# Kernel tuning notes

Measured on AMD Instinct MI355X. Metric: run time of the kernel, lower is better.

Reference implementation:

```python
import jax, jax.numpy as jnp
import numpy as np
import math

B, N, C = 16, 4096, 256
WS = 8            # window_size
NH = 8            # num_heads
HD = C // NH      # head_dim = 32
LK = 32           # linformer compressed length
G = 16            # global bank tokens


def setup_inputs() -> dict:
    key = jax.random.key(0)
    ks = jax.random.split(key, 10)
    x = jax.random.normal(ks[0], (B, N, C), dtype=jnp.float32)
    W_qkv = jax.random.normal(ks[1], (C, 3 * C), dtype=jnp.float32) * 0.02
    b_qkv = jnp.zeros((3 * C,), dtype=jnp.float32)
    E_k = jax.random.normal(ks[2], (WS * WS, LK), dtype=jnp.float32) * 0.02
    E_v = jax.random.normal(ks[3], (WS * WS, LK), dtype=jnp.float32) * 0.02
    k_bank = jax.random.normal(ks[4], (G, C), dtype=jnp.float32)
    v_bank = jax.random.normal(ks[5], (G, C), dtype=jnp.float32)
    W_proj = jax.random.normal(ks[6], (C, C), dtype=jnp.float32) * 0.02
    b_proj = jnp.zeros((C,), dtype=jnp.float32)
    return {"x": x, "W_qkv": W_qkv, "b_qkv": b_qkv, "E_k": E_k, "E_v": E_v,
            "k_bank": k_bank, "v_bank": v_bank, "W_proj": W_proj, "b_proj": b_proj,
            "window_size": WS, "num_heads": NH}


def reference(x, W_qkv, b_qkv, E_k, E_v, k_bank, v_bank, W_proj, b_proj, window_size, num_heads):
    Bb, Nn, Cc = x.shape
    Hs = int(math.isqrt(Nn))          # H = W = sqrt(N), divisible by window_size here
    ws = window_size
    nh = Hs // ws                      # windows per side
    hd = Cc // num_heads
    NW = ws * ws                       # tokens per window

    # ---- window partition: [B,N,C] -> [BW, NW, C]
    xw = x.reshape(Bb, nh, ws, nh, ws, Cc).transpose(0, 1, 3, 2, 4, 5)
    xw = xw.reshape(Bb * nh * nh, NW, Cc)
    BW = xw.shape[0]

    # ---- qkv projection and head split: (3, BW, H, NW, hd)
    qkv = (xw @ W_qkv + b_qkv).reshape(BW, NW, 3, num_heads, hd)
    qkv = qkv.transpose(2, 0, 3, 1, 4)
    q, k, v = qkv[0], qkv[1], qkv[2]

    # ---- Linformer KV compression: NW == seq_len (no pad branch)
    k_c = jnp.einsum('nk,bhnd->bhkd', E_k, k)   # [BW,H,LK,hd]
    v_c = jnp.einsum('nk,bhnd->bhkd', E_v, v)

    # ---- global memory bank, broadcast to all windows: [BW,H,G,hd]
    Gt = k_bank.shape[0]
    kb = jnp.broadcast_to(k_bank.reshape(Gt, num_heads, hd).transpose(1, 0, 2)[None],
                          (BW, num_heads, Gt, hd))
    vb = jnp.broadcast_to(v_bank.reshape(Gt, num_heads, hd).transpose(1, 0, 2)[None],
                          (BW, num_heads, Gt, hd))

    k_full = jnp.concatenate([k_c, kb], axis=2)  # [BW,H,LK+G,hd]
    v_full = jnp.concatenate([v_c, vb], axis=2)

    # ---- SDPA (dropout_p = 0)
    scale = 1.0 / math.sqrt(hd)
    scores = jnp.einsum('bhqd,bhkd->bhqk', q, k_full) * scale
    attn = jax.nn.softmax(scores, axis=-1)
    out = jnp.einsum('bhqk,bhkd->bhqd', attn, v_full)     # [BW,H,NW,hd]

    out = out.transpose(0, 2, 1, 3).reshape(BW, NW, Cc)
    out = out @ W_proj + b_proj

    # ---- window reverse: [BW,NW,C] -> [B,N,C]
    out = out.reshape(Bb, nh, nh, ws, ws, Cc).transpose(0, 1, 3, 2, 4, 5)
    out = out.reshape(Bb, Hs * Hs, Cc)
    return out
```

## Files before the change

kernel.cpp:

```cpp
#include <hip/hip_runtime.h>
#include <hip/hip_bf16.h>


typedef unsigned int uint;
typedef __attribute__((ext_vector_type(8))) short short8;
typedef __attribute__((ext_vector_type(4))) float f32x4;
typedef __attribute__((ext_vector_type(4))) uint uintx4;

__device__ __forceinline__ float bup(uint hs) {
    return __uint_as_float(hs << 16);
}
__device__ __forceinline__ uint f2b(float f) {
    __hip_bfloat16 h = __float2bfloat16(f);
    unsigned short u;
    __builtin_memcpy(&u, &h, 2);
    return (uint)u;
}
__device__ __forceinline__ uint f2b2(float a, float b) {
    __hip_bfloat162 h = __float22bfloat162_rn(make_float2(a, b));
    uint u;
    __builtin_memcpy(&u, &h, 4);
    return u;
}
__device__ __forceinline__ f32x4 mfma16(short8 a, short8 b, f32x4 c) {
    return __builtin_amdgcn_mfma_f32_16x16x32_bf16(a, b, c, 0, 0, 0);
}
__device__ __forceinline__ int sw256(int r, int c) { return r * 256 + (c ^ ((r & 7) << 3)); }

__device__ __forceinline__ short8 xpose(f32x4 a, f32x4 b, float s, int lane) {
    const uint pa0 = f2b2(a[0] * s, a[1] * s), pa1 = f2b2(a[2] * s, a[3] * s);
    const uint pb0 = f2b2(b[0] * s, b[1] * s), pb1 = f2b2(b[2] * s, b[3] * s);
    const int s0 = ((lane >> 4) & 1) * 32 + (lane & 15);
    const int s1 = s0 + 16;
    const uint w0a = __shfl(pa0, s0), w0b = __shfl(pb0, s0);
    const uint w1a = __shfl(pa1, s0), w1b = __shfl(pb1, s0);
    const uint w2a = __shfl(pa0, s1), w2b = __shfl(pb0, s1);
    const uint w3a = __shfl(pa1, s1), w3b = __shfl(pb1, s1);
    const bool hi = lane >= 32;
    uintx4 u;
    u[0] = hi ? w0b : w0a;
    u[1] = hi ? w1b : w1a;
    u[2] = hi ? w2b : w2a;
    u[3] = hi ? w3b : w3a;
    short8 r;
    __builtin_memcpy(&r, &u, 16);
    return r;
}

#define WS_WHQ 0
#define WS_WHP 196608
#define WS_WLP 262144
#define WS_EKT 327680
#define WS_EVT 329728
#define WS_KBF 331776
#define WS_VBF 335872

__global__ void __launch_bounds__(256)
eswa_prep(const float* __restrict__ Wqkv, const float* __restrict__ Wproj,
          const float* __restrict__ Ek, const float* __restrict__ Ev,
          const float* __restrict__ kbank, const float* __restrict__ vbank,
          short* __restrict__ wsp)
{
    const int blk = blockIdx.x, thr = threadIdx.x;
    if (blk < 192) {
        const int jh = blk & 1;
        const int g = (blk >> 1) * 256 + thr;
        const int lane = g & 63, tk = (g >> 6) & 7, tn = g >> 9;
        const int quad = lane >> 4, l16 = lane & 15;
        const int c = tn * 16 + l16;
        const int r0 = tk * 32 + quad * 8 + jh * 4;
        const float w0 = Wqkv[(r0 + 0) * 768 + c], w1 = Wqkv[(r0 + 1) * 768 + c];
        const float w2 = Wqkv[(r0 + 2) * 768 + c], w3 = Wqkv[(r0 + 3) * 768 + c];
        *(uint2*)(wsp + WS_WHQ + ((tn * 8 + tk) * 64 + lane) * 8 + jh * 4) =
            make_uint2(f2b2(w0, w1), f2b2(w2, w3));
    } else if (blk < 256) {
        const int idx = blk - 192, jh = idx & 1;
        const int g = (idx >> 1) * 256 + thr;
        const int lane = g & 63, tk = (g >> 6) & 7, tn = g >> 9;
        const int quad = lane >> 4, l16 = lane & 15;
        const int c = tn * 16 + l16;
        const int r0 = tk * 32 + quad * 8 + jh * 4;
        float w[4];
        #pragma unroll
        for (int j = 0; j < 4; ++j) w[j] = Wproj[(r0 + j) * 256 + c];
        const uint h01 = f2b2(w[0], w[1]), h23 = f2b2(w[2], w[3]);
        const float l0 = w[0] - bup(h01 & 0xffffu), l1 = w[1] - bup(h01 >> 16);
        const float l2 = w[2] - bup(h23 & 0xffffu), l3 = w[3] - bup(h23 >> 16);
        const int o = ((tn * 8 + tk) * 64 + lane) * 8 + jh * 4;
        *(uint2*)(wsp + WS_WHP + o) = make_uint2(h01, h23);
        *(uint2*)(wsp + WS_WLP + o) = make_uint2(f2b2(l0, l1), f2b2(l2, l3));
    } else if (blk < 258) {
        const float* E = (blk == 256) ? Ek : Ev;
        const int base = (blk == 256) ? WS_EKT : WS_EVT;
        const int lane = thr & 63, tk = (thr >> 6) & 1, tm = (thr >> 7) & 1;
        const int quad = lane >> 4, l16 = lane & 15;
        const int lk = tm * 16 + l16;
        uint pk[4];
        #pragma unroll
        for (int jp = 0; jp < 4; ++jp) {
            const int t = tk * 32 + quad * 8 + jp * 2;
            pk[jp] = f2b2(E[t * 32 + lk], E[(t + 1) * 32 + lk]);
        }
        *(uint4*)(wsp + base + ((tm * 2 + tk) * 64 + lane) * 8) =
            make_uint4(pk[0], pk[1], pk[2], pk[3]);
    } else {
        for (int idx = thr; idx < 512; idx += 256) {
            const int hh = idx >> 6, l = idx & 63;
            const int l16 = l & 15, q = l >> 4;
            uint pk[4];
            #pragma unroll
            for (int jp = 0; jp < 4; ++jp)
                pk[jp] = f2b2(kbank[l16 * 256 + hh * 32 + q * 8 + jp * 2],
                              kbank[l16 * 256 + hh * 32 + q * 8 + jp * 2 + 1]);
            *(uint4*)(wsp + WS_KBF + idx * 8) = make_uint4(pk[0], pk[1], pk[2], pk[3]);
        }
        for (int idx = thr; idx < 1024; idx += 256) {
            const int hh = idx >> 7, md = (idx >> 6) & 1, l = idx & 63;
            const int l16 = l & 15, q = l >> 4;
            uint pk[4] = {0u, 0u, 0u, 0u};
            if (q < 2) {
                #pragma unroll
                for (int jp = 0; jp < 4; ++jp)
                    pk[jp] = f2b2(vbank[(q * 8 + jp * 2) * 256 + hh * 32 + md * 16 + l16],
                                  vbank[(q * 8 + jp * 2 + 1) * 256 + hh * 32 + md * 16 + l16]);
            }
            *(uint4*)(wsp + WS_VBF + idx * 8) = make_uint4(pk[0], pk[1], pk[2], pk[3]);
        }
    }
}

#define SMEM_BYTES 65536

__global__ void __launch_bounds__(512, 4)
eswa_main(const float* __restrict__ x, const float* __restrict__ bqkv,
          const float* __restrict__ bproj, const short* __restrict__ wsp,
          float* __restrict__ out)
{
    extern __shared__ char smem[];
    short* xh   = (short*)smem;
    short* attn = (short*)smem + 16384;

    const int tid  = threadIdx.x;
    const int wave = tid >> 6;
    const int lane = tid & 63;
    const int quad = lane >> 4;
    const int l16  = lane & 15;
    const int h    = wave;

    const int b  = blockIdx.x >> 6;
    const int w  = blockIdx.x & 63;
    const int rw = w >> 3;
    const int cw = w & 7;

    #pragma unroll
    for (int i = 0; i < 8; ++i) {
        const int vi = tid + 512 * i;
        const int t  = vi >> 6;
        const int c  = (vi & 63) * 4;
        const int n  = (rw * 8 + (t >> 3)) * 64 + cw * 8 + (t & 7);
        const float4 xv = *(const float4*)(x + (size_t)(b * 4096 + n) * 256 + c);
        *(uint2*)(xh + sw256(t, c)) = make_uint2(f2b2(xv.x, xv.y), f2b2(xv.z, xv.w));
    }
    __syncthreads();

    const short* WF = wsp + WS_WHQ;

    short8 kfr[2][2], vfr[2][2];
    {
        f32x4 acc[2][4];
        #pragma unroll
        for (int nd = 0; nd < 2; ++nd) {
            const float bk = bqkv[256 + h * 32 + nd * 16 + l16];
            #pragma unroll
            for (int mt = 0; mt < 4; ++mt) acc[nd][mt] = (f32x4){bk, bk, bk, bk};
        }
        #pragma unroll 2
        for (int tk = 0; tk < 8; ++tk) {
            short8 xf[4];
            #pragma unroll
            for (int mt = 0; mt < 4; ++mt)
                xf[mt] = *(const short8*)(xh + sw256(mt * 16 + l16, tk * 32 + quad * 8));
            #pragma unroll
            for (int nd = 0; nd < 2; ++nd) {
                const short8 wf =
                    *(const short8*)(WF + (((16 + h * 2 + nd) * 8 + tk) * 64 + lane) * 8);
                #pragma unroll
                for (int mt = 0; mt < 4; ++mt) acc[nd][mt] = mfma16(xf[mt], wf, acc[nd][mt]);
            }
        }
        #pragma unroll
        for (int nd = 0; nd < 2; ++nd)
            #pragma unroll
            for (int kk = 0; kk < 2; ++kk)
                kfr[nd][kk] = xpose(acc[nd][2 * kk], acc[nd][2 * kk + 1], 1.0f, lane);
    }
    {
        f32x4 acc[2][4];
        #pragma unroll
        for (int nd = 0; nd < 2; ++nd) {
            const float bv = bqkv[512 + h * 32 + nd * 16 + l16];
            #pragma unroll
            for (int mt = 0; mt < 4; ++mt) acc[nd][mt] = (f32x4){bv, bv, bv, bv};
        }
        #pragma unroll 2
        for (int tk = 0; tk < 8; ++tk) {
            short8 xf[4];
            #pragma unroll
            for (int mt = 0; mt < 4; ++mt)
                xf[mt] = *(const short8*)(xh + sw256(mt * 16 + l16, tk * 32 + quad * 8));
            #pragma unroll
            for (int nd = 0; nd < 2; ++nd) {
                const short8 wf =
                    *(const short8*)(WF + (((32 + h * 2 + nd) * 8 + tk) * 64 + lane) * 8);
                #pragma unroll
                for (int mt = 0; mt < 4; ++mt) acc[nd][mt] = mfma16(xf[mt], wf, acc[nd][mt]);
            }
        }
        #pragma unroll
        for (int nd = 0; nd < 2; ++nd)
            #pragma unroll
            for (int kk = 0; kk < 2; ++kk)
                vfr[nd][kk] = xpose(acc[nd][2 * kk], acc[nd][2 * kk + 1], 1.0f, lane);
    }
    short8 kcf[2], vcf[2];
    {
        short8 ekf[2][2], evf[2][2];
        #pragma unroll
        for (int tm = 0; tm < 2; ++tm)
            #pragma unroll
            for (int kk = 0; kk < 2; ++kk) {
                ekf[tm][kk] = *(const short8*)(wsp + WS_EKT + ((tm * 2 + kk) * 64 + lane) * 8);
                evf[tm][kk] = *(const short8*)(wsp + WS_EVT + ((tm * 2 + kk) * 64 + lane) * 8);
            }
        f32x4 ck[2][2];
        #pragma unroll
        for (int md = 0; md < 2; ++md)
            #pragma unroll
            for (int nl = 0; nl < 2; ++nl) ck[md][nl] = (f32x4){0, 0, 0, 0};
        #pragma unroll
        for (int kk = 0; kk < 2; ++kk)
            #pragma unroll
            for (int md = 0; md < 2; ++md)
                #pragma unroll
                for (int nl = 0; nl < 2; ++nl)
                    ck[md][nl] = mfma16(kfr[md][kk], ekf[nl][kk], ck[md][nl]);
        #pragma unroll
        for (int nl = 0; nl < 2; ++nl)
            kcf[nl] = xpose(ck[0][nl], ck[1][nl], 1.0f, lane);
        f32x4 cv[2][2];
        #pragma unroll
        for (int ml = 0; ml < 2; ++ml)
            #pragma unroll
            for (int nd = 0; nd < 2; ++nd) cv[ml][nd] = (f32x4){0, 0, 0, 0};
        #pragma unroll
        for (int kk = 0; kk < 2; ++kk)
            #pragma unroll
            for (int ml = 0; ml < 2; ++ml)
                #pragma unroll
                for (int nd = 0; nd < 2; ++nd)
                    cv[ml][nd] = mfma16(evf[ml][kk], vfr[nd][kk], cv[ml][nd]);
        #pragma unroll
        for (int nd = 0; nd < 2; ++nd)
            vcf[nd] = xpose(cv[0][nd], cv[1][nd], 1.0f, lane);
    }
    const short8 kbf = *(const short8*)(wsp + WS_KBF + (h * 64 + lane) * 8);
    short8 vbf[2];
    #pragma unroll
    for (int md = 0; md < 2; ++md)
        vbf[md] = *(const short8*)(wsp + WS_VBF + ((h * 2 + md) * 64 + lane) * 8);

    short8 qfr[4];
    {
        f32x4 acc[2][4];
        #pragma unroll
        for (int md = 0; md < 2; ++md) {
            const float4 bq = *(const float4*)(bqkv + h * 32 + md * 16 + quad * 4);
            #pragma unroll
            for (int nt = 0; nt < 4; ++nt) acc[md][nt] = (f32x4){bq.x, bq.y, bq.z, bq.w};
        }
        #pragma unroll 2
        for (int tk = 0; tk < 8; ++tk) {
            short8 xf[4];
            #pragma unroll
            for (int nt = 0; nt < 4; ++nt)
                xf[nt] = *(const short8*)(xh + sw256(nt * 16 + l16, tk * 32 + quad * 8));
            #pragma unroll
            for (int md = 0; md < 2; ++md) {
                const short8 wf =
                    *(const short8*)(WF + (((h * 2 + md) * 8 + tk) * 64 + lane) * 8);
                #pragma unroll
                for (int nt = 0; nt < 4; ++nt) acc[md][nt] = mfma16(wf, xf[nt], acc[md][nt]);
            }
        }
        #pragma unroll
        for (int nt = 0; nt < 4; ++nt)
            qfr[nt] = xpose(acc[0][nt], acc[1][nt], 0.17677669529663687f, lane);
    }
    __syncthreads();

    short* scr = (short*)smem + wave * 2048;
    if (lane >= 32) {
        *(uint4*)(scr + (1 * 64 + lane) * 8) = make_uint4(0, 0, 0, 0);
        *(uint4*)(scr + (3 * 64 + lane) * 8) = make_uint4(0, 0, 0, 0);
    }

    #pragma unroll
    for (int th = 0; th < 2; ++th) {
        f32x4 sc[2][3];
        #pragma unroll
        for (int mt = 0; mt < 2; ++mt) {
            const short8 qa = qfr[th * 2 + mt];
            sc[mt][0] = mfma16(qa, kcf[0], (f32x4){0, 0, 0, 0});
            sc[mt][1] = mfma16(qa, kcf[1], (f32x4){0, 0, 0, 0});
            sc[mt][2] = mfma16(qa, kbf,    (f32x4){0, 0, 0, 0});
        }
        float inv[2][4];
        #pragma unroll
        for (int mt = 0; mt < 2; ++mt) {
            #pragma unroll
            for (int r = 0; r < 4; ++r) {
                float mm = fmaxf(fmaxf(sc[mt][0][r], sc[mt][1][r]), sc[mt][2][r]);
                mm = fmaxf(mm, __shfl_xor(mm, 1));
                mm = fmaxf(mm, __shfl_xor(mm, 2));
                mm = fmaxf(mm, __shfl_xor(mm, 4));
                mm = fmaxf(mm, __shfl_xor(mm, 8));
                const float e0 = __expf(sc[mt][0][r] - mm);
                const float e1 = __expf(sc[mt][1][r] - mm);
                const float e2 = __expf(sc[mt][2][r] - mm);
                sc[mt][0][r] = e0; sc[mt][1][r] = e1; sc[mt][2][r] = e2;
                float su = e0 + e1 + e2;
                su += __shfl_xor(su, 1);
                su += __shfl_xor(su, 2);
                su += __shfl_xor(su, 4);
                su += __shfl_xor(su, 8);
                inv[mt][r] = 1.0f / su;
            }
        }
        #pragma unroll
        for (int mt = 0; mt < 2; ++mt)
            #pragma unroll
            for (int nk = 0; nk < 3; ++nk) {
                const int qt = (nk * 2 + (l16 >> 3)) & 3;
                const int base = (mt * 2 + (nk >> 1)) * 64 + qt * 16 + quad * 4;
                #pragma unroll
                for (int r = 0; r < 4; ++r)
                    scr[(base + r) * 8 + (l16 & 7)] =
                        (short)f2b(sc[mt][nk][r] * inv[mt][r]);
            }
        asm volatile("s_waitcnt lgkmcnt(0)" ::: "memory");
        __builtin_amdgcn_sched_barrier(0);
        short8 pa[2][2];
        #pragma unroll
        for (int mt = 0; mt < 2; ++mt)
            #pragma unroll
            for (int kk = 0; kk < 2; ++kk)
                pa[mt][kk] = *(const short8*)(scr + ((mt * 2 + kk) * 64 + lane) * 8);
        #pragma unroll
        for (int mt = 0; mt < 2; ++mt)
            #pragma unroll
            for (int md = 0; md < 2; ++md) {
                f32x4 o = mfma16(vcf[md], pa[mt][0], (f32x4){0, 0, 0, 0});
                o = mfma16(vbf[md], pa[mt][1], o);
                *(uint2*)(attn + sw256((th * 2 + mt) * 16 + l16,
                                       h * 32 + md * 16 + quad * 4)) =
                    make_uint2(f2b2(o[0], o[1]), f2b2(o[2], o[3]));
            }
    }
    __syncthreads();

    {
        const short* Whp = wsp + WS_WHP;
        const short* Wlp = wsp + WS_WLP;
        f32x4 acc[2][4];
        #pragma unroll
        for (int p = 0; p < 2; ++p) {
            const float bi = bproj[(wave * 2 + p) * 16 + l16];
            #pragma unroll
            for (int m = 0; m < 4; ++m) acc[p][m] = (f32x4){bi, bi, bi, bi};
        }
        #pragma unroll 2
        for (int tk = 0; tk < 8; ++tk) {
            short8 aA[4];
            #pragma unroll
            for (int m = 0; m < 4; ++m)
                aA[m] = *(const short8*)(attn + sw256(m * 16 + l16, tk * 32 + quad * 8));
            #pragma unroll
            for (int p = 0; p < 2; ++p) {
                const int bo = (((wave * 2 + p) * 8 + tk) * 64 + lane) * 8;
                const short8 bh = *(const short8*)(Whp + bo);
                const short8 bl = *(const short8*)(Wlp + bo);
                #pragma unroll
                for (int m = 0; m < 4; ++m) {
                    acc[p][m] = mfma16(aA[m], bh, acc[p][m]);
                    acc[p][m] = mfma16(aA[m], bl, acc[p][m]);
                }
            }
        }
        #pragma unroll
        for (int p = 0; p < 2; ++p)
            #pragma unroll
            for (int m = 0; m < 4; ++m)
                #pragma unroll
                for (int r = 0; r < 4; ++r) {
                    const int t = m * 16 + quad * 4 + r;
                    const int n = (rw * 8 + (t >> 3)) * 64 + cw * 8 + (t & 7);
                    out[(size_t)(b * 4096 + n) * 256 + (wave * 2 + p) * 16 + l16] =
                        acc[p][m][r];
                }
    }
}

extern "C" void kernel_launch(void* const* d_in, const int* in_sizes, int n_in,
                              void* d_out, int out_size, void* d_ws, size_t ws_size,
                              hipStream_t stream) {
    const float* x     = (const float*)d_in[0];
    const float* Wqkv  = (const float*)d_in[1];
    const float* bqkv  = (const float*)d_in[2];
    const float* Ek    = (const float*)d_in[3];
    const float* Ev    = (const float*)d_in[4];
    const float* kbank = (const float*)d_in[5];
    const float* vbank = (const float*)d_in[6];
    const float* Wproj = (const float*)d_in[7];
    const float* bproj = (const float*)d_in[8];
    float* outp        = (float*)d_out;
    short* wsp         = (short*)d_ws;
    (void)in_sizes; (void)n_in; (void)out_size; (void)ws_size;

    (void)hipFuncSetAttribute((const void*)eswa_main,
                              hipFuncAttributeMaxDynamicSharedMemorySize, SMEM_BYTES);

    eswa_prep<<<259, 256, 0, stream>>>(Wqkv, Wproj, Ek, Ev, kbank, vbank, wsp);
    eswa_main<<<1024, 512, SMEM_BYTES, stream>>>(x, bqkv, bproj, wsp, outp);
}
```

Before: 187.8 us.

## Fuse QKV projections over half-width x tiles to cut shared memory and raise occupancy

Loads x into shared memory in two 128-channel halves and computes Q, K and V projections together in one pass, sharing the x fragment loads across all three. Shared memory drops from 64KB to 48KB, launch bounds rise to 6 blocks per SM, and the per-wave softmax scratch is halved and XOR-swizzled so it is processed one m-tile at a time. In exchange, all three projection accumulators stay live at once, which raises register pressure and may force spills under the tighter launch bound. It also adds an extra barrier between the two x halves.

```diff
diff --git a/kernel.cpp b/kernel.cpp
--- a/kernel.cpp
+++ b/kernel.cpp
@@ -26,6 +26,7 @@
     return __builtin_amdgcn_mfma_f32_16x16x32_bf16(a, b, c, 0, 0, 0);
 }
 __device__ __forceinline__ int sw256(int r, int c) { return r * 256 + (c ^ ((r & 7) << 3)); }
+__device__ __forceinline__ int sw128(int r, int c) { return r * 128 + (c ^ ((r & 7) << 3)); }
 
 __device__ __forceinline__ short8 xpose(f32x4 a, f32x4 b, float s, int lane) {
     const uint pa0 = f2b2(a[0] * s, a[1] * s), pa1 = f2b2(a[2] * s, a[3] * s);
@@ -129,16 +130,16 @@
     }
 }
 
-#define SMEM_BYTES 65536
-
-__global__ void __launch_bounds__(512, 4)
+#define SMEM_BYTES 49152
+
+__global__ void __launch_bounds__(512, 6)
 eswa_main(const float* __restrict__ x, const float* __restrict__ bqkv,
           const float* __restrict__ bproj, const short* __restrict__ wsp,
           float* __restrict__ out)
 {
     extern __shared__ char smem[];
     short* xh   = (short*)smem;
-    short* attn = (short*)smem + 16384;
+    short* attn = (short*)smem + 8192;
 
     const int tid  = threadIdx.x;
     const int wave = tid >> 6;
@@ -152,76 +153,84 @@
     const int rw = w >> 3;
     const int cw = w & 7;
 
-    #pragma unroll
-    for (int i = 0; i < 8; ++i) {
-        const int vi = tid + 512 * i;
-        const int t  = vi >> 6;
-        const int c  = (vi & 63) * 4;
-        const int n  = (rw * 8 + (t >> 3)) * 64 + cw * 8 + (t & 7);
-        const float4 xv = *(const float4*)(x + (size_t)(b * 4096 + n) * 256 + c);
-        *(uint2*)(xh + sw256(t, c)) = make_uint2(f2b2(xv.x, xv.y), f2b2(xv.z, xv.w));
+    const short* WF = wsp + WS_WHQ;
+
+    f32x4 kacc[2][4], vacc[2][4], qacc[2][4];
+    #pragma unroll
+    for (int nd = 0; nd < 2; ++nd) {
+        const float bk = bqkv[256 + h * 32 + nd * 16 + l16];
+        const float bv = bqkv[512 + h * 32 + nd * 16 + l16];
+        #pragma unroll
+        for (int mt = 0; mt < 4; ++mt) {
+            kacc[nd][mt] = (f32x4){bk, bk, bk, bk};
+            vacc[nd][mt] = (f32x4){bv, bv, bv, bv};
+        }
+    }
+    #pragma unroll
+    for (int md = 0; md < 2; ++md) {
+        const float4 bq = *(const float4*)(bqkv + h * 32 + md * 16 + quad * 4);
+        #pragma unroll
+        for (int nt = 0; nt < 4; ++nt) qacc[md][nt] = (f32x4){bq.x, bq.y, bq.z, bq.w};
+    }
+
+    for (int hf = 0; hf < 2; ++hf) {
+        if (hf) __syncthreads();
+        #pragma unroll
+        for (int i = 0; i < 4; ++i) {
+            const int vi = tid + 512 * i;
+            const int t  = vi >> 5;
+            const int cl = (vi & 31) * 4;
+            const int n  = (rw * 8 + (t >> 3)) * 64 + cw * 8 + (t & 7);
+            const float4 xv =
+                *(const float4*)(x + (size_t)(b * 4096 + n) * 256 + hf * 128 + cl);
+            *(uint2*)(xh + sw128(t, cl)) = make_uint2(f2b2(xv.x, xv.y), f2b2(xv.z, xv.w));
+        }
+        __syncthreads();
+        #pragma unroll
+        for (int t4 = 0; t4 < 4; ++t4) {
+            const int tk = hf * 4 + t4;
+            short8 xf[4];
+            #pragma unroll
+            for (int mt = 0; mt < 4; ++mt)
+                xf[mt] = *(const short8*)(xh + sw128(mt * 16 + l16, t4 * 32 + quad * 8));
+            #pragma unroll
+            for (int nd = 0; nd < 2; ++nd) {
+                const short8 wk =
+                    *(const short8*)(WF + (((16 + h * 2 + nd) * 8 + tk) * 64 + lane) * 8);
+                #pragma unroll
+                for (int mt = 0; mt < 4; ++mt) kacc[nd][mt] = mfma16(xf[mt], wk, kacc[nd][mt]);
+            }
+            #pragma unroll
+            for (int nd = 0; nd < 2; ++nd) {
+                const short8 wv =
+                    *(const short8*)(WF + (((32 + h * 2 + nd) * 8 + tk) * 64 + lane) * 8);
+                #pragma unroll
+                for (int mt = 0; mt < 4; ++mt) vacc[nd][mt] = mfma16(xf[mt], wv, vacc[nd][mt]);
+            }
+            #pragma unroll
+            for (int md = 0; md < 2; ++md) {
+                const short8 wq =
+                    *(const short8*)(WF + (((h * 2 + md) * 8 + tk) * 64 + lane) * 8);
+                #pragma unroll
+                for (int nt = 0; nt < 4; ++nt) qacc[md][nt] = mfma16(wq, xf[nt], qacc[md][nt]);
+            }
+        }
     }
     __syncthreads();
 
-    const short* WF = wsp + WS_WHQ;
-
     short8 kfr[2][2], vfr[2][2];
-    {
-        f32x4 acc[2][4];
-        #pragma unroll
-        for (int nd = 0; nd < 2; ++nd) {
-            const float bk = bqkv[256 + h * 32 + nd * 16 + l16];
-            #pragma unroll
-            for (int mt = 0; mt < 4; ++mt) acc[nd][mt] = (f32x4){bk, bk, bk, bk};
-        }
-        #pragma unroll 2
-        for (int tk = 0; tk < 8; ++tk) {
-            short8 xf[4];
-            #pragma unroll
-            for (int mt = 0; mt < 4; ++mt)
-                xf[mt] = *(const short8*)(xh + sw256(mt * 16 + l16, tk * 32 + quad * 8));
-            #pragma unroll
-            for (int nd = 0; nd < 2; ++nd) {
-                const short8 wf =
-                    *(const short8*)(WF + (((16 + h * 2 + nd) * 8 + tk) * 64 + lane) * 8);
-                #pragma unroll
-                for (int mt = 0; mt < 4; ++mt) acc[nd][mt] = mfma16(xf[mt], wf, acc[nd][mt]);
-            }
-        }
-        #pragma unroll
-        for (int nd = 0; nd < 2; ++nd)
-            #pragma unroll
-            for (int kk = 0; kk < 2; ++kk)
-                kfr[nd][kk] = xpose(acc[nd][2 * kk], acc[nd][2 * kk + 1], 1.0f, lane);
-    }
-    {
-        f32x4 acc[2][4];
-        #pragma unroll
-        for (int nd = 0; nd < 2; ++nd) {
-            const float bv = bqkv[512 + h * 32 + nd * 16 + l16];
-            #pragma unroll
-            for (int mt = 0; mt < 4; ++mt) acc[nd][mt] = (f32x4){bv, bv, bv, bv};
-        }
-        #pragma unroll 2
-        for (int tk = 0; tk < 8; ++tk) {
-            short8 xf[4];
-            #pragma unroll
-            for (int mt = 0; mt < 4; ++mt)
-                xf[mt] = *(const short8*)(xh + sw256(mt * 16 + l16, tk * 32 + quad * 8));
-            #pragma unroll
-            for (int nd = 0; nd < 2; ++nd) {
-                const short8 wf =
-                    *(const short8*)(WF + (((32 + h * 2 + nd) * 8 + tk) * 64 + lane) * 8);
-                #pragma unroll
-                for (int mt = 0; mt < 4; ++mt) acc[nd][mt] = mfma16(xf[mt], wf, acc[nd][mt]);
-            }
-        }
-        #pragma unroll
-        for (int nd = 0; nd < 2; ++nd)
-            #pragma unroll
-            for (int kk = 0; kk < 2; ++kk)
-                vfr[nd][kk] = xpose(acc[nd][2 * kk], acc[nd][2 * kk + 1], 1.0f, lane);
-    }
+    #pragma unroll
+    for (int nd = 0; nd < 2; ++nd)
+        #pragma unroll
+        for (int kk = 0; kk < 2; ++kk) {
+            kfr[nd][kk] = xpose(kacc[nd][2 * kk], kacc[nd][2 * kk + 1], 1.0f, lane);
+            vfr[nd][kk] = xpose(vacc[nd][2 * kk], vacc[nd][2 * kk + 1], 1.0f, lane);
+        }
+    short8 qfr[4];
+    #pragma unroll
+    for (int nt = 0; nt < 4; ++nt)
+        qfr[nt] = xpose(qacc[0][nt], qacc[1][nt], 0.17677669529663687f, lane);
+
     short8 kcf[2], vcf[2];
     {
         short8 ekf[2][2], evf[2][2];
@@ -269,40 +278,13 @@
     for (int md = 0; md < 2; ++md)
         vbf[md] = *(const short8*)(wsp + WS_VBF + ((h * 2 + md) * 64 + lane) * 8);
 
-    short8 qfr[4];
-    {
-        f32x4 acc[2][4];
-        #pragma unroll
-        for (int md = 0; md < 2; ++md) {
-            const float4 bq = *(const float4*)(bqkv + h * 32 + md * 16 + quad * 4);
-            #pragma unroll
-            for (int nt = 0; nt < 4; ++nt) acc[md][nt] = (f32x4){bq.x, bq.y, bq.z, bq.w};
-        }
-        #pragma unroll 2
-        for (int tk = 0; tk < 8; ++tk) {
-            short8 xf[4];
-            #pragma unroll
-            for (int nt = 0; nt < 4; ++nt)
-                xf[nt] = *(const short8*)(xh + sw256(nt * 16 + l16, tk * 32 + quad * 8));
-            #pragma unroll
-            for (int md = 0; md < 2; ++md) {
-                const short8 wf =
-                    *(const short8*)(WF + (((h * 2 + md) * 8 + tk) * 64 + lane) * 8);
-                #pragma unroll
-                for (int nt = 0; nt < 4; ++nt) acc[md][nt] = mfma16(wf, xf[nt], acc[md][nt]);
-            }
-        }
-        #pragma unroll
-        for (int nt = 0; nt < 4; ++nt)
-            qfr[nt] = xpose(acc[0][nt], acc[1][nt], 0.17677669529663687f, lane);
-    }
-    __syncthreads();
-
-    short* scr = (short*)smem + wave * 2048;
+    short* scr = (short*)smem + wave * 1024;
     if (lane >= 32) {
-        *(uint4*)(scr + (1 * 64 + lane) * 8) = make_uint4(0, 0, 0, 0);
-        *(uint4*)(scr + (3 * 64 + lane) * 8) = make_uint4(0, 0, 0, 0);
-    }
+        const int ch = (64 + lane) ^ ((lane >> 3) & 7);
+        *(uint4*)(scr + ch * 8) = make_uint4(0, 0, 0, 0);
+    }
+    const int rdx0 = (lane ^ ((lane >> 3) & 7)) * 8;
+    const int rdx1 = ((64 + lane) ^ ((lane >> 3) & 7)) * 8;
 
     #pragma unroll
     for (int th = 0; th < 2; ++th) {
@@ -337,34 +319,31 @@
             }
         }
         #pragma unroll
-        for (int mt = 0; mt < 2; ++mt)
+        for (int mt = 0; mt < 2; ++mt) {
             #pragma unroll
             for (int nk = 0; nk < 3; ++nk) {
                 const int qt = (nk * 2 + (l16 >> 3)) & 3;
-                const int base = (mt * 2 + (nk >> 1)) * 64 + qt * 16 + quad * 4;
-                #pragma unroll
-                for (int r = 0; r < 4; ++r)
-                    scr[(base + r) * 8 + (l16 & 7)] =
-                        (short)f2b(sc[mt][nk][r] * inv[mt][r]);
-            }
-        asm volatile("s_waitcnt lgkmcnt(0)" ::: "memory");
-        __builtin_amdgcn_sched_barrier(0);
-        short8 pa[2][2];
-        #pragma unroll
-        for (int mt = 0; mt < 2; ++mt)
-            #pragma unroll
-            for (int kk = 0; kk < 2; ++kk)
-                pa[mt][kk] = *(const short8*)(scr + ((mt * 2 + kk) * 64 + lane) * 8);
-        #pragma unroll
-        for (int mt = 0; mt < 2; ++mt)
+                const int kk = nk >> 1;
+                const int xr = (qt * 2 + (quad >> 1)) & 7;
+                #pragma unroll
+                for (int r = 0; r < 4; ++r) {
+                    const int ch = (kk * 64 + qt * 16 + quad * 4 + r) ^ xr;
+                    scr[ch * 8 + (l16 & 7)] = (short)f2b(sc[mt][nk][r] * inv[mt][r]);
+                }
+            }
+            asm volatile("s_waitcnt lgkmcnt(0)" ::: "memory");
+            __builtin_amdgcn_sched_barrier(0);
+            const short8 pa0 = *(const short8*)(scr + rdx0);
+            const short8 pa1 = *(const short8*)(scr + rdx1);
             #pragma unroll
             for (int md = 0; md < 2; ++md) {
-                f32x4 o = mfma16(vcf[md], pa[mt][0], (f32x4){0, 0, 0, 0});
-                o = mfma16(vbf[md], pa[mt][1], o);
+                f32x4 o = mfma16(vcf[md], pa0, (f32x4){0, 0, 0, 0});
+                o = mfma16(vbf[md], pa1, o);
                 *(uint2*)(attn + sw256((th * 2 + mt) * 16 + l16,
                                        h * 32 + md * 16 + quad * 4)) =
                     make_uint2(f2b2(o[0], o[1]), f2b2(o[2], o[3]));
             }
+        }
     }
     __syncthreads();
 
```

Measured after the change: 652.5 us. 3.47x slower.
